# Kernel optimization log

Hardware: AMD Instinct MI355X
Metric: run time of the kernel (lower is better)

Reference implementation:

```python
import math
import jax, jax.numpy as jnp
import numpy as np

B, W, C = 2, 2048, 1024
N, K = 16, 64  # heads, head dim (C // N)


def setup_inputs() -> dict:
    key = jax.random.key(0)
    ks = jax.random.split(key, 6)
    return {
        "in_sequence_bwc": jax.random.normal(ks[0], (B, W, C), dtype=jnp.float32),
        "W_proj": jax.random.normal(ks[1], (C, C), dtype=jnp.float32) * (1.0 / math.sqrt(C)),
        "b_proj": jax.random.normal(ks[2], (C,), dtype=jnp.float32) * 0.01,
        "generators_1nwk": jax.random.normal(ks[3], (1, N, W, K), dtype=jnp.float32),
        "W_mix": jax.random.normal(ks[4], (C, C), dtype=jnp.float32) * (1.0 / math.sqrt(C)),
        "b_mix": jax.random.normal(ks[5], (C,), dtype=jnp.float32) * 0.01,
    }


def reference(in_sequence_bwc, W_proj, b_proj, generators_1nwk, W_mix, b_mix):
    b, w, c = in_sequence_bwc.shape
    # shared projection (torch Linear: x @ W.T + b)
    p_bwc = in_sequence_bwc @ W_proj.T + b_proj
    p_bnwk = p_bwc.reshape(b, w, N, K).transpose(0, 2, 1, 3)  # [b, n, w, k]
    g_nwk = generators_1nwk[0, :, :w, :]  # [n, w, k]
    # data-dependent metric generator: p^T @ G -> [b, n, k, k]
    m_bnkk = jnp.einsum("bnwk,nwl->bnkl", p_bnwk, g_nwk)
    tril_kk = jnp.tril(jnp.ones((K, K), dtype=in_sequence_bwc.dtype))
    m_bnkk = m_bnkk * tril_kk  # lower-triangular mask on k x k
    m_bnkk = m_bnkk @ jnp.swapaxes(m_bnkk, -1, -2)  # PSD metric M M^T
    # bilinear scores: P @ M @ P^T, scaled
    pm_bnwk = jnp.einsum("bnwk,bnkl->bnwl", p_bnwk, m_bnkk)
    scores_bnww = jnp.einsum("bnwk,bnvk->bnwv", pm_bnwk, p_bnwk) / math.sqrt(K)
    causal = jnp.tril(jnp.ones((w, w), dtype=bool))
    scores_bnww = jnp.where(causal, scores_bnww, -jnp.inf)
    attn_bnww = jax.nn.softmax(scores_bnww, axis=-1)
    nudged_bnwk = attn_bnww @ p_bnwk
    nudged_bwc = nudged_bnwk.transpose(0, 2, 1, 3).reshape(b, w, c)
    return nudged_bwc @ W_mix.T + b_mix
```

## Files before the change

kernel.cpp:

```cpp
#include <hip/hip_runtime.h>
#include <math.h>

#define B_  2
#define W_  2048
#define C_  1024
#define NH_ 16
#define KD_ 64

__device__ __forceinline__ int sw(int r, int c) {
    return (r << 6) + ((((c >> 2) ^ ((r >> 2) & 7)) << 2) | (c & 3));
}

__device__ __forceinline__ void stage64s(const float* __restrict__ src,
                                         float* dst, int tid) {
#pragma unroll
    for (int q = 0; q < 4; ++q) {
        int idx = tid + (q << 8);
        int r   = idx >> 4;
        int c   = (idx & 15) << 2;
        *(float4*)&dst[sw(r, c)] = *(const float4*)(src + (idx << 2));
    }
}

__device__ __forceinline__ void stage64(const float* __restrict__ src,
                                        float (*dst)[68], int tid) {
#pragma unroll
    for (int q = 0; q < 4; ++q) {
        int idx = tid + (q << 8);
        int e   = idx << 2;
        int r   = e >> 6;
        int c   = e & 63;
        *(float4*)&dst[r][c] = *(const float4*)(src + e);
    }
}

template<int OUT_P_LAYOUT>
__global__ __launch_bounds__(256, 2)
void gemm_nt(const float* __restrict__ A, const float* __restrict__ Bw,
             const float* __restrict__ bias, float* __restrict__ Cout)
{
    __shared__ float As[16][68];
    __shared__ float Bs[16][68];
    const int tid = threadIdx.x;
    const int tx  = tid & 15, ty = tid >> 4;
    const int m0  = blockIdx.x << 6;
    const int n0  = blockIdx.y << 6;
    const int lrow = tid >> 2;
    const int lkq  = (tid & 3) << 2;
    const float* Ap = A  + (size_t)(m0 + lrow) * C_ + lkq;
    const float* Bp = Bw + (size_t)(n0 + lrow) * C_ + lkq;

    float acc[4][4] = {};
    for (int k0 = 0; k0 < C_; k0 += 16) {
        float4 av = *(const float4*)(Ap + k0);
        float4 bv = *(const float4*)(Bp + k0);
        __syncthreads();
        As[lkq+0][lrow] = av.x; As[lkq+1][lrow] = av.y;
        As[lkq+2][lrow] = av.z; As[lkq+3][lrow] = av.w;
        Bs[lkq+0][lrow] = bv.x; Bs[lkq+1][lrow] = bv.y;
        Bs[lkq+2][lrow] = bv.z; Bs[lkq+3][lrow] = bv.w;
        __syncthreads();
#pragma unroll
        for (int kk = 0; kk < 16; ++kk) {
            float4 a4 = *(const float4*)&As[kk][ty << 2];
            float4 b4 = *(const float4*)&Bs[kk][tx << 2];
            float am[4] = {a4.x, a4.y, a4.z, a4.w};
            float bm[4] = {b4.x, b4.y, b4.z, b4.w};
#pragma unroll
            for (int i = 0; i < 4; ++i)
#pragma unroll
                for (int j = 0; j < 4; ++j)
                    acc[i][j] = fmaf(am[i], bm[j], acc[i][j]);
        }
    }

    const int gc = n0 + (tx << 2);
    float4 bb = *(const float4*)&bias[gc];
#pragma unroll
    for (int i = 0; i < 4; ++i) {
        int gm = m0 + (ty << 2) + i;
        float4 o;
        o.x = acc[i][0] + bb.x;
        o.y = acc[i][1] + bb.y;
        o.z = acc[i][2] + bb.z;
        o.w = acc[i][3] + bb.w;
        if (OUT_P_LAYOUT) {
            int b = gm >> 11;
            int w = gm & 2047;
            int n = gc >> 6;
            int k = gc & 63;
            *(float4*)(Cout + (((size_t)(b * NH_ + n) * W_ + w) * KD_ + k)) = o;
        } else {
            *(float4*)(Cout + (size_t)gm * C_ + gc) = o;
        }
    }
}

__global__ __launch_bounds__(256, 2)
void metric_part(const float* __restrict__ p, const float* __restrict__ g,
                 float* __restrict__ part)
{
    __shared__ float Ps[32][68];
    __shared__ float Gs[32][68];
    const int ch  = blockIdx.x;
    const int bn  = blockIdx.y;
    const int n   = bn & (NH_ - 1);
    const int tid = threadIdx.x;
    const int tx  = tid & 15, ty = tid >> 4;
    const float* pb = p + (size_t)bn * W_ * KD_ + (size_t)(ch << 8) * KD_;
    const float* gb = g + (size_t)n  * W_ * KD_ + (size_t)(ch << 8) * KD_;

    float acc[4][4] = {};
    for (int w0 = 0; w0 < 256; w0 += 32) {
        __syncthreads();
#pragma unroll
        for (int q = 0; q < 2; ++q) {
            int idx = tid + (q << 8);
            int e   = idx << 2;
            int r   = e >> 6;
            int c   = e & 63;
            *(float4*)&Ps[r][c] = *(const float4*)(pb + (size_t)(w0 + r) * KD_ + c);
            *(float4*)&Gs[r][c] = *(const float4*)(gb + (size_t)(w0 + r) * KD_ + c);
        }
        __syncthreads();
#pragma unroll 8
        for (int w = 0; w < 32; ++w) {
            float4 a4 = *(const float4*)&Ps[w][ty << 2];
            float4 b4 = *(const float4*)&Gs[w][tx << 2];
            float am[4] = {a4.x, a4.y, a4.z, a4.w};
            float bm[4] = {b4.x, b4.y, b4.z, b4.w};
#pragma unroll
            for (int i = 0; i < 4; ++i)
#pragma unroll
                for (int j = 0; j < 4; ++j)
                    acc[i][j] = fmaf(am[i], bm[j], acc[i][j]);
        }
    }

    float* ob = part + (size_t)(bn * 8 + ch) * KD_ * KD_;
#pragma unroll
    for (int i = 0; i < 4; ++i) {
        float4 o; o.x = acc[i][0]; o.y = acc[i][1]; o.z = acc[i][2]; o.w = acc[i][3];
        *(float4*)(ob + ((ty << 2) + i) * KD_ + (tx << 2)) = o;
    }
}

__global__ __launch_bounds__(256, 2)
void metric_reduce(const float* __restrict__ part, float* __restrict__ m2)
{
    __shared__ float M1s[64][68];
    const int bn  = blockIdx.x;
    const int tid = threadIdx.x;
    const int tx  = tid & 15, ty = tid >> 4;
    const float* pb = part + (size_t)bn * 8 * KD_ * KD_;

#pragma unroll
    for (int v = 0; v < 4; ++v) {
        int f = tid + (v << 8);
        int e = f << 2;
        float4 s = *(const float4*)(pb + e);
#pragma unroll
        for (int c = 1; c < 8; ++c) {
            float4 t = *(const float4*)(pb + c * 4096 + e);
            s.x += t.x; s.y += t.y; s.z += t.z; s.w += t.w;
        }
        int k = e >> 6, l = e & 63;
        if (l + 0 > k) s.x = 0.f;
        if (l + 1 > k) s.y = 0.f;
        if (l + 2 > k) s.z = 0.f;
        if (l + 3 > k) s.w = 0.f;
        *(float4*)&M1s[k][l] = s;
    }
    __syncthreads();

    float a2[4][4] = {};
#pragma unroll
    for (int jq = 0; jq < 64; jq += 4) {
        float4 av[4], bv[4];
#pragma unroll
        for (int i = 0; i < 4; ++i) av[i] = *(const float4*)&M1s[(ty << 2) + i][jq];
#pragma unroll
        for (int j = 0; j < 4; ++j) bv[j] = *(const float4*)&M1s[(tx << 2) + j][jq];
#pragma unroll
        for (int i = 0; i < 4; ++i)
#pragma unroll
            for (int j = 0; j < 4; ++j)
                a2[i][j] += av[i].x * bv[j].x + av[i].y * bv[j].y +
                            av[i].z * bv[j].z + av[i].w * bv[j].w;
    }

    float* ob = m2 + (size_t)bn * KD_ * KD_;
#pragma unroll
    for (int i = 0; i < 4; ++i) {
        float4 o; o.x = a2[i][0]; o.y = a2[i][1]; o.z = a2[i][2]; o.w = a2[i][3];
        *(float4*)(ob + ((ty << 2) + i) * KD_ + (tx << 2)) = o;
    }
}

__global__ __launch_bounds__(256, 2)
void qgen_k(const float* __restrict__ p, const float* __restrict__ m2,
            float* __restrict__ qout)
{
    __shared__ float Pt[64][68];
    __shared__ float Ms[64][68];
    const int bn  = blockIdx.y;
    const int w0  = blockIdx.x << 6;
    const int tid = threadIdx.x;
    const int tx  = tid & 15, ty = tid >> 4;
    const float* pb = p  + (size_t)bn * W_ * KD_ + (size_t)w0 * KD_;
    const float* mb = m2 + (size_t)bn * KD_ * KD_;

    stage64(pb, Pt, tid);
    stage64(mb, Ms, tid);
    __syncthreads();

    float acc[4][4] = {};
#pragma unroll
    for (int kq = 0; kq < 64; kq += 4) {
        float4 av[4];
        float  bm[4][4];
#pragma unroll
        for (int i = 0; i < 4; ++i) av[i] = *(const float4*)&Pt[(ty << 2) + i][kq];
#pragma unroll
        for (int kk = 0; kk < 4; ++kk) {
            float4 t = *(const float4*)&Ms[kq + kk][tx << 2];
            bm[kk][0] = t.x; bm[kk][1] = t.y; bm[kk][2] = t.z; bm[kk][3] = t.w;
        }
#pragma unroll
        for (int i = 0; i < 4; ++i) {
            float am[4] = {av[i].x, av[i].y, av[i].z, av[i].w};
#pragma unroll
            for (int j = 0; j < 4; ++j)
                acc[i][j] = fmaf(am[0], bm[0][j],
                            fmaf(am[1], bm[1][j],
                            fmaf(am[2], bm[2][j],
                            fmaf(am[3], bm[3][j], acc[i][j]))));
        }
    }

    float* ob = qout + (size_t)bn * W_ * KD_ + (size_t)w0 * KD_;
#pragma unroll
    for (int i = 0; i < 4; ++i) {
        float4 o;
        o.x = acc[i][0] * 0.125f; o.y = acc[i][1] * 0.125f;
        o.z = acc[i][2] * 0.125f; o.w = acc[i][3] * 0.125f;
        *(float4*)(ob + ((ty << 2) + i) * KD_ + (tx << 2)) = o;
    }
}

__global__ __launch_bounds__(256, 2)
void attn_k(const float* __restrict__ qg, const float* __restrict__ p,
            float* __restrict__ nud)
{
    __shared__ float Qs[4096];
    __shared__ float Ks[2][4096];
    __shared__ float Es[4096];
    const int bid = blockIdx.x;
    const int bn  = bid & 31;
    const int qt  = (bid < 512) ? (31 - (bid >> 5)) : ((bid - 512) >> 5);
    const int b   = bn >> 4, n = bn & 15;
    const int tid = threadIdx.x;
    const int tx  = tid & 15, ty = tid >> 4;
    const float* qb = qg + (size_t)bn * W_ * KD_ + (size_t)(qt << 6) * KD_;
    const float* kb = p  + (size_t)bn * W_ * KD_;

    stage64s(qb, Qs, tid);
    stage64s(kb, Ks[0], tid);
    __syncthreads();

    float acc[4][4] = {};
    float mi[4], li[4];
#pragma unroll
    for (int i = 0; i < 4; ++i) { mi[i] = -INFINITY; li[i] = 0.f; }

    float4 ld[4];

    for (int j0 = 0; j0 <= qt; ++j0) {
        const int cur = j0 & 1;
        const float* Kc = Ks[cur];

        if (j0 < qt) {
            const float* nx = kb + (size_t)((j0 + 1) << 6) * KD_;
#pragma unroll
            for (int q = 0; q < 4; ++q)
                ld[q] = *(const float4*)(nx + ((tid + (q << 8)) << 2));
        }

        float s[4][4] = {};
        __builtin_amdgcn_s_setprio(1);
#pragma unroll
        for (int kq = 0; kq < 16; ++kq) {
            float4 av[4], bv[4];
#pragma unroll
            for (int i = 0; i < 4; ++i)
                av[i] = *(const float4*)&Qs[sw((ty << 2) + i, kq << 2)];
#pragma unroll
            for (int j = 0; j < 4; ++j)
                bv[j] = *(const float4*)&Kc[sw((tx << 2) + j, kq << 2)];
#pragma unroll
            for (int i = 0; i < 4; ++i)
#pragma unroll
                for (int j = 0; j < 4; ++j)
                    s[i][j] = fmaf(av[i].x, bv[j].x,
                              fmaf(av[i].y, bv[j].y,
                              fmaf(av[i].z, bv[j].z,
                              fmaf(av[i].w, bv[j].w, s[i][j]))));
        }
        __builtin_amdgcn_s_setprio(0);

        if (j0 == qt) {
#pragma unroll
            for (int i = 0; i < 4; ++i)
#pragma unroll
                for (int j = 0; j < 4; ++j)
                    if (((tx << 2) + j) > ((ty << 2) + i)) s[i][j] = -INFINITY;
        }

        float mnew[4], al[4];
#pragma unroll
        for (int i = 0; i < 4; ++i) {
            float rm = fmaxf(fmaxf(s[i][0], s[i][1]), fmaxf(s[i][2], s[i][3]));
            rm = fmaxf(rm, __shfl_xor(rm, 1, 16));
            rm = fmaxf(rm, __shfl_xor(rm, 2, 16));
            rm = fmaxf(rm, __shfl_xor(rm, 4, 16));
            rm = fmaxf(rm, __shfl_xor(rm, 8, 16));
            mnew[i] = fmaxf(mi[i], rm);
        }
#pragma unroll
        for (int i = 0; i < 4; ++i) {
#pragma unroll
            for (int j = 0; j < 4; ++j) s[i][j] = __expf(s[i][j] - mnew[i]);
            float rs = s[i][0] + s[i][1] + s[i][2] + s[i][3];
            rs += __shfl_xor(rs, 1, 16);
            rs += __shfl_xor(rs, 2, 16);
            rs += __shfl_xor(rs, 4, 16);
            rs += __shfl_xor(rs, 8, 16);
            al[i] = __expf(mi[i] - mnew[i]);
            li[i] = li[i] * al[i] + rs;
            mi[i] = mnew[i];
        }

#pragma unroll
        for (int i = 0; i < 4; ++i) {
            float4 e; e.x = s[i][0]; e.y = s[i][1]; e.z = s[i][2]; e.w = s[i][3];
            *(float4*)&Es[sw((ty << 2) + i, tx << 2)] = e;
#pragma unroll
            for (int j = 0; j < 4; ++j) acc[i][j] *= al[i];
        }

        if (j0 < qt) {
            float* Kn = (float*)Ks[cur ^ 1];
#pragma unroll
            for (int q = 0; q < 4; ++q) {
                int idx = tid + (q << 8);
                *(float4*)&Kn[sw(idx >> 4, (idx & 15) << 2)] = ld[q];
            }
        }

        __builtin_amdgcn_s_setprio(1);
#pragma unroll
        for (int jq = 0; jq < 64; jq += 4) {
            float4 av[4];
            float  vm[4][4];
#pragma unroll
            for (int i = 0; i < 4; ++i) av[i] = *(const float4*)&Es[sw((ty << 2) + i, jq)];
#pragma unroll
            for (int kk = 0; kk < 4; ++kk) {
                float4 t = *(const float4*)&Kc[sw(jq + kk, tx << 2)];
                vm[kk][0] = t.x; vm[kk][1] = t.y; vm[kk][2] = t.z; vm[kk][3] = t.w;
            }
#pragma unroll
            for (int i = 0; i < 4; ++i) {
                float am[4] = {av[i].x, av[i].y, av[i].z, av[i].w};
#pragma unroll
                for (int c = 0; c < 4; ++c)
                    acc[i][c] = fmaf(am[0], vm[0][c],
                                fmaf(am[1], vm[1][c],
                                fmaf(am[2], vm[2][c],
                                fmaf(am[3], vm[3][c], acc[i][c]))));
            }
        }
        __builtin_amdgcn_s_setprio(0);

        __syncthreads();
    }

    const int wrow = qt << 6;
#pragma unroll
    for (int i = 0; i < 4; ++i) {
        float inv = 1.f / li[i];
        float4 o;
        o.x = acc[i][0] * inv; o.y = acc[i][1] * inv;
        o.z = acc[i][2] * inv; o.w = acc[i][3] * inv;
        size_t row = (size_t)(b * W_ + wrow + (ty << 2) + i);
        *(float4*)(nud + row * C_ + (n << 6) + (tx << 2)) = o;
    }
}

extern "C" void kernel_launch(void* const* d_in, const int* in_sizes, int n_in,
                              void* d_out, int out_size, void* d_ws, size_t ws_size,
                              hipStream_t stream)
{
    (void)in_sizes; (void)n_in; (void)out_size; (void)ws_size;
    const float* X  = (const float*)d_in[0];
    const float* Wp = (const float*)d_in[1];
    const float* bp = (const float*)d_in[2];
    const float* G  = (const float*)d_in[3];
    const float* Wm = (const float*)d_in[4];
    const float* bm = (const float*)d_in[5];
    float* out = (float*)d_out;
    float* ws  = (float*)d_ws;

    float* Pbuf = ws;
    float* Qbuf = ws + 4194304;
    float* M2   = ws + 8388608;
    float* Nud  = ws + 8519680;
    float* Part = Qbuf;

    dim3 blk(256);
    gemm_nt<1>   <<<dim3(64, 16), blk, 0, stream>>>(X, Wp, bp, Pbuf);
    metric_part  <<<dim3(8, 32),  blk, 0, stream>>>(Pbuf, G, Part);
    metric_reduce<<<dim3(32),     blk, 0, stream>>>(Part, M2);
    qgen_k       <<<dim3(32, 32), blk, 0, stream>>>(Pbuf, M2, Qbuf);
    attn_k       <<<dim3(1024),   blk, 0, stream>>>(Qbuf, Pbuf, Nud);
    gemm_nt<0>   <<<dim3(64, 16), blk, 0, stream>>>(Nud, Wm, bm, out);
}
```

Measured before the change: 793.5 us.

## Halve attention query tile to 32 rows and double grid size

The attention kernel now processes 32 query rows per block instead of 64. Each thread holds 2x4 outputs, and the grid doubles to 2048 blocks, ordered by descending causal extent. Shared memory per block shrinks and launch bounds are raised to 3 blocks per SM, which is meant to improve occupancy and load balance across the causal triangle. In exchange, each K tile is loaded twice as often per query row, so arithmetic intensity per LDS/global load is lower.

Measured after the change: 786.9 us. No clear change (-0.8%).

```diff
diff --git a/kernel.cpp b/kernel.cpp
--- a/kernel.cpp
+++ b/kernel.cpp
@@ -248,57 +248,64 @@
     }
 }
 
-__global__ __launch_bounds__(256, 2)
+__global__ __launch_bounds__(256, 3)
 void attn_k(const float* __restrict__ qg, const float* __restrict__ p,
             float* __restrict__ nud)
 {
-    __shared__ float Qs[4096];
+    __shared__ float Qs[2048];
     __shared__ float Ks[2][4096];
-    __shared__ float Es[4096];
-    const int bid = blockIdx.x;
-    const int bn  = bid & 31;
-    const int qt  = (bid < 512) ? (31 - (bid >> 5)) : ((bid - 512) >> 5);
-    const int b   = bn >> 4, n = bn & 15;
-    const int tid = threadIdx.x;
-    const int tx  = tid & 15, ty = tid >> 4;
-    const float* qb = qg + (size_t)bn * W_ * KD_ + (size_t)(qt << 6) * KD_;
+    __shared__ float Es[2048];
+    const int bid  = blockIdx.x;
+    const int bn   = bid & 31;
+    const int t    = 63 - (bid >> 5);
+    const int jmax = t >> 1;
+    const int b    = bn >> 4, n = bn & 15;
+    const int tid  = threadIdx.x;
+    const int tx   = tid & 15, ty = tid >> 4;
+    const int roff = (t & 1) << 5;
+    const float* qb = qg + (size_t)bn * W_ * KD_ + (size_t)(t << 5) * KD_;
     const float* kb = p  + (size_t)bn * W_ * KD_;
 
-    stage64s(qb, Qs, tid);
+#pragma unroll
+    for (int q = 0; q < 2; ++q) {
+        int idx = tid + (q << 8);
+        int r = idx >> 4, c = (idx & 15) << 2;
+        *(float4*)&Qs[sw(r, c)] = *(const float4*)(qb + (idx << 2));
+    }
     stage64s(kb, Ks[0], tid);
     __syncthreads();
 
-    float acc[4][4] = {};
-    float mi[4], li[4];
-#pragma unroll
-    for (int i = 0; i < 4; ++i) { mi[i] = -INFINITY; li[i] = 0.f; }
+    float acc[2][4] = {};
+    float mi[2], li[2];
+#pragma unroll
+    for (int i = 0; i < 2; ++i) { mi[i] = -INFINITY; li[i] = 0.f; }
 
     float4 ld[4];
 
-    for (int j0 = 0; j0 <= qt; ++j0) {
+    for (int j0 = 0; j0 <= jmax; ++j0) {
         const int cur = j0 & 1;
         const float* Kc = Ks[cur];
 
-        if (j0 < qt) {
+        if (j0 < jmax) {
             const float* nx = kb + (size_t)((j0 + 1) << 6) * KD_;
 #pragma unroll
             for (int q = 0; q < 4; ++q)
                 ld[q] = *(const float4*)(nx + ((tid + (q << 8)) << 2));
         }
 
-        float s[4][4] = {};
+        float s[2][4] = {};
         __builtin_amdgcn_s_setprio(1);
 #pragma unroll
         for (int kq = 0; kq < 16; ++kq) {
-            float4 av[4], bv[4];
-#pragma unroll
-            for (int i = 0; i < 4; ++i)
-                av[i] = *(const float4*)&Qs[sw((ty << 2) + i, kq << 2)];
+            float4 av[2], bv[4];
+#pragma unroll
+            for (int i = 0; i < 2; ++i)
+                av[i] = *(const float4*)&Qs[sw((ty << 1) + i, kq << 2)];
 #pragma unroll
             for (int j = 0; j < 4; ++j)
                 bv[j] = *(const float4*)&Kc[sw((tx << 2) + j, kq << 2)];
 #pragma unroll
-            for (int i = 0; i < 4; ++i)
+            for (int i = 0; i < 2; ++i)
 #pragma unroll
                 for (int j = 0; j < 4; ++j)
                     s[i][j] = fmaf(av[i].x, bv[j].x,
@@ -308,17 +315,17 @@
         }
         __builtin_amdgcn_s_setprio(0);
 
-        if (j0 == qt) {
-#pragma unroll
-            for (int i = 0; i < 4; ++i)
+        if (j0 == jmax) {
+#pragma unroll
+            for (int i = 0; i < 2; ++i)
 #pragma unroll
                 for (int j = 0; j < 4; ++j)
-                    if (((tx << 2) + j) > ((ty << 2) + i)) s[i][j] = -INFINITY;
-        }
-
-        float mnew[4], al[4];
-#pragma unroll
-        for (int i = 0; i < 4; ++i) {
+                    if (((tx << 2) + j) > (roff + (ty << 1) + i)) s[i][j] = -INFINITY;
+        }
+
+        float mnew[2], al[2];
+#pragma unroll
+        for (int i = 0; i < 2; ++i) {
             float rm = fmaxf(fmaxf(s[i][0], s[i][1]), fmaxf(s[i][2], s[i][3]));
             rm = fmaxf(rm, __shfl_xor(rm, 1, 16));
             rm = fmaxf(rm, __shfl_xor(rm, 2, 16));
@@ -327,7 +334,7 @@
             mnew[i] = fmaxf(mi[i], rm);
         }
 #pragma unroll
-        for (int i = 0; i < 4; ++i) {
+        for (int i = 0; i < 2; ++i) {
 #pragma unroll
             for (int j = 0; j < 4; ++j) s[i][j] = __expf(s[i][j] - mnew[i]);
             float rs = s[i][0] + s[i][1] + s[i][2] + s[i][3];
@@ -341,14 +348,14 @@
         }
 
 #pragma unroll
-        for (int i = 0; i < 4; ++i) {
+        for (int i = 0; i < 2; ++i) {
             float4 e; e.x = s[i][0]; e.y = s[i][1]; e.z = s[i][2]; e.w = s[i][3];
-            *(float4*)&Es[sw((ty << 2) + i, tx << 2)] = e;
+            *(float4*)&Es[sw((ty << 1) + i, tx << 2)] = e;
 #pragma unroll
             for (int j = 0; j < 4; ++j) acc[i][j] *= al[i];
         }
 
-        if (j0 < qt) {
+        if (j0 < jmax) {
             float* Kn = (float*)Ks[cur ^ 1];
 #pragma unroll
             for (int q = 0; q < 4; ++q) {
@@ -360,17 +367,18 @@
         __builtin_amdgcn_s_setprio(1);
 #pragma unroll
         for (int jq = 0; jq < 64; jq += 4) {
-            float4 av[4];
+            float4 av[2];
             float  vm[4][4];
 #pragma unroll
-            for (int i = 0; i < 4; ++i) av[i] = *(const float4*)&Es[sw((ty << 2) + i, jq)];
+            for (int i = 0; i < 2; ++i)
+                av[i] = *(const float4*)&Es[sw((ty << 1) + i, jq)];
 #pragma unroll
             for (int kk = 0; kk < 4; ++kk) {
-                float4 t = *(const float4*)&Kc[sw(jq + kk, tx << 2)];
-                vm[kk][0] = t.x; vm[kk][1] = t.y; vm[kk][2] = t.z; vm[kk][3] = t.w;
+                float4 tv = *(const float4*)&Kc[sw(jq + kk, tx << 2)];
+                vm[kk][0] = tv.x; vm[kk][1] = tv.y; vm[kk][2] = tv.z; vm[kk][3] = tv.w;
             }
 #pragma unroll
-            for (int i = 0; i < 4; ++i) {
+            for (int i = 0; i < 2; ++i) {
                 float am[4] = {av[i].x, av[i].y, av[i].z, av[i].w};
 #pragma unroll
                 for (int c = 0; c < 4; ++c)
@@ -385,14 +393,14 @@
         __syncthreads();
     }
 
-    const int wrow = qt << 6;
-#pragma unroll
-    for (int i = 0; i < 4; ++i) {
+    const int wrow = t << 5;
+#pragma unroll
+    for (int i = 0; i < 2; ++i) {
         float inv = 1.f / li[i];
         float4 o;
         o.x = acc[i][0] * inv; o.y = acc[i][1] * inv;
         o.z = acc[i][2] * inv; o.w = acc[i][3] * inv;
-        size_t row = (size_t)(b * W_ + wrow + (ty << 2) + i);
+        size_t row = (size_t)(b * W_ + wrow + (ty << 1) + i);
         *(float4*)(nud + row * C_ + (n << 6) + (tx << 2)) = o;
     }
 }
@@ -422,6 +430,6 @@
     metric_part  <<<dim3(8, 32),  blk, 0, stream>>>(Pbuf, G, Part);
     metric_reduce<<<dim3(32),     blk, 0, stream>>>(Part, M2);
     qgen_k       <<<dim3(32, 32), blk, 0, stream>>>(Pbuf, M2, Qbuf);
-    attn_k       <<<dim3(1024),   blk, 0, stream>>>(Qbuf, Pbuf, Nud);
+    attn_k       <<<dim3(2048),   blk, 0, stream>>>(Qbuf, Pbuf, Nud);
     gemm_nt<0>   <<<dim3(64, 16), blk, 0, stream>>>(Nud, Wm, bm, out);
 }
```
